# Performance work log

Measured on AMD Instinct MI355X. Metric: run time of the kernel, lower is better.

Reference implementation:

```python
import jax, jax.numpy as jnp
import numpy as np

EPS = 1e-6
DROPOUT_RATE = 0.1
NEG_INF = -1e9


def _rmsnorm(x, scale):
    # Llama2-style RMSNorm over the last (head_dim) axis.
    x_rms = jnp.sqrt((x * x).mean(axis=-1, keepdims=True) + EPS)
    return (x / x_rms) * scale


def setup_inputs() -> dict:
    key = jax.random.key(0)
    ks = jax.random.split(key, 5)
    B, S, H, D = 2, 2048, 16, 128
    query = jax.random.normal(ks[0], (B, S, H, D), dtype=jnp.float32)
    k_ = jax.random.normal(ks[1], (B, S, H, D), dtype=jnp.float32)
    value = jax.random.normal(ks[2], (B, S, H, D), dtype=jnp.float32)
    # Causal attention bias, broadcastable to [B, H, Sq, Sk].
    causal = jnp.tril(jnp.ones((S, S), dtype=bool))
    bias = jnp.where(causal, 0.0, NEG_INF).astype(jnp.float32)[None, None, :, :]
    q_scale = jnp.ones((D,), dtype=jnp.float32)
    k_scale = jnp.ones((D,), dtype=jnp.float32)
    # Dropout keep mask: broadcast over q dimension (dropout_shape[-2] = 1).
    keep_mask = jax.random.bernoulli(ks[3], 1.0 - DROPOUT_RATE, (B, H, 1, S))
    return {
        "query": query,
        "key": k_,
        "value": value,
        "bias": bias,
        "q_scale": q_scale,
        "k_scale": k_scale,
        "keep_mask": keep_mask,
    }


def reference(query, key, value, bias, q_scale, k_scale, keep_mask):
    # QK RMSNorm (maxtext applies RMSNorm to q and k inside attention).
    q = _rmsnorm(query, q_scale)  # [B, Sq, H, D]
    k = _rmsnorm(key, k_scale)    # [B, Sk, H, D]
    # Attention logits [B, H, Sq, Sk] (no 1/sqrt(d) scaling in this module).
    attn_weights = jnp.einsum("bqhd,bkhd->bhqk", q, k)
    attn_weights = attn_weights + bias.astype(attn_weights.dtype)
    attn_weights = jax.nn.softmax(attn_weights, axis=-1)
    # Dropout with keep mask broadcast over q length.
    keep_prob = 1.0 - DROPOUT_RATE
    multiplier = keep_mask.astype(attn_weights.dtype) / jnp.asarray(keep_prob, dtype=attn_weights.dtype)
    attn_weights = attn_weights * multiplier
    # Weighted value combine -> [B, Sq, H, D].
    return jnp.einsum("bhqk,bkhd->bqhd", attn_weights, value)
```

## Files before the change

kernel.cpp:

```cpp
#include <hip/hip_runtime.h>
#include <stdint.h>

typedef unsigned short u16;
typedef __attribute__((ext_vector_type(8))) _Float16 half8;
typedef __attribute__((ext_vector_type(4))) float f32x4;

#define DEVI __device__ __forceinline__

constexpr int B_ = 2, S_ = 2048, H_ = 16, D_ = 128;
constexpr int BH_ = B_ * H_;
constexpr float EPS_ = 1e-6f;
constexpr float INV_KEEP = 1.0f / 0.9f;

constexpr size_t Q_OFF = 0;
constexpr size_t K_OFF = (size_t)BH_ * S_ * D_ * 2;
constexpr size_t V_OFF = 2 * K_OFF;

DEVI u16 f16b(float x) { union { _Float16 f; u16 u; } c; c.f = (_Float16)x; return c.u; }

DEVI void gload16(const char* g, char* l) {
  __builtin_amdgcn_global_load_lds((const __attribute__((address_space(1))) uint32_t*)g,
                                   (__attribute__((address_space(3))) uint32_t*)l, 16, 0, 0);
}

__global__ __launch_bounds__(256) void k_norm(const float* __restrict__ q,
                                              const float* __restrict__ k,
                                              const float* __restrict__ qs,
                                              const float* __restrict__ ks,
                                              char* __restrict__ ws) {
  const int lane32 = threadIdx.x & 31;
  const int half = threadIdx.x >> 5;
  const float4 sq = *(const float4*)(qs + lane32 * 4);
  const float4 sk = *(const float4*)(ks + lane32 * 4);
  const int NROW = 2 * B_ * S_ * H_;

  for (int row = blockIdx.x * 8 + half; row < NROW; row += gridDim.x * 8) {
    const bool isQ = row < NROW / 2;
    const int r2 = isQ ? row : row - NROW / 2;
    const int b = r2 >> 15;
    const int s = (r2 >> 4) & (S_ - 1);
    const int h = r2 & 15;
    const float4 v = *(const float4*)((isQ ? q : k) + (size_t)r2 * D_ + lane32 * 4);
    float ss = v.x * v.x + v.y * v.y + v.z * v.z + v.w * v.w;
    ss += __shfl_xor(ss, 16); ss += __shfl_xor(ss, 8); ss += __shfl_xor(ss, 4);
    ss += __shfl_xor(ss, 2);  ss += __shfl_xor(ss, 1);
    const float f = rsqrtf(ss * (1.0f / D_) + EPS_);
    const float4 sc = isQ ? sq : sk;
    ushort4 o;
    o.x = f16b(v.x * f * sc.x); o.y = f16b(v.y * f * sc.y);
    o.z = f16b(v.z * f * sc.z); o.w = f16b(v.w * f * sc.w);
    const int bh = b * H_ + h;
    if (isQ) {
      *(ushort4*)(ws + Q_OFF + (((size_t)bh * S_ + s) * D_ + lane32 * 4) * 2) = o;
    } else {
      const int kt = s >> 6, r = s & 63;
      const int off = (r * 256 + lane32 * 8) ^ ((r & 7) << 4);
      *(ushort4*)(ws + K_OFF + ((size_t)(bh * 32 + kt) << 14) + off) = o;
    }
  }
}

__global__ __launch_bounds__(256) void k_vt(const float* __restrict__ v,
                                            const void* __restrict__ mask,
                                            char* __restrict__ ws) {
  __shared__ __align__(16) u16 tile[64][132];
  __shared__ float mlds[64];
  __shared__ int mode;

  const int bid = blockIdx.x;
  const int bh = bid >> 5, st = bid & 31;
  const int b = bh >> 4, h = bh & 15;
  const int t = threadIdx.x;

  if (t == 0) {
    const uint32_t* mw = (const uint32_t*)mask;
    bool all01 = true, allf = true;
    for (int i = 0; i < 64; i++) {
      uint32_t w = mw[i];
      if (w != 0u && w != 1u) all01 = false;
      if (w != 0u && w != 0x3F800000u) allf = false;
    }
    mode = all01 ? 1 : (allf ? 2 : 0);
  }
  __syncthreads();
  if (t < 64) {
    const int kidx = bh * S_ + st * 64 + t;
    int bit;
    if (mode == 1)      bit = ((const int*)mask)[kidx] != 0;
    else if (mode == 2) bit = ((const float*)mask)[kidx] != 0.0f;
    else                bit = ((const uint8_t*)mask)[kidx] != 0;
    mlds[t] = bit ? INV_KEEP : 0.0f;
  }
  __syncthreads();

  const int r = t >> 2, sub = t & 3;
  const size_t base = ((size_t)(b * S_ + st * 64 + r) * H_ + h) * D_;
  const float m = mlds[r];
  #pragma unroll
  for (int j = 0; j < 8; j++) {
    const int d = sub * 32 + j * 4;
    float4 val = *(const float4*)(v + base + d);
    ushort4 o;
    o.x = f16b(val.x * m); o.y = f16b(val.y * m);
    o.z = f16b(val.z * m); o.w = f16b(val.w * m);
    *(ushort4*)&tile[r][d] = o;
  }
  __syncthreads();

  const int dg = t >> 5;
  const int w = t & 31;
  char* tbase = ws + V_OFF + ((size_t)(bh * 32 + st) << 14);
  #pragma unroll
  for (int rr = 0; rr < 16; rr++) {
    const int d = rr * 8 + dg;
    const uint32_t word = (uint32_t)tile[2 * w][d] | ((uint32_t)tile[2 * w + 1][d] << 16);
    const int off = (d * 128 + w * 4) ^ ((d & 7) << 4);
    *(uint32_t*)(tbase + off) = word;
  }
}

__global__ __launch_bounds__(256, 2) void k_attn(const char* __restrict__ ws,
                                                 float* __restrict__ out) {
  __shared__ __align__(16) u16 K0[8192], V0[8192];
  __shared__ __align__(16) u16 K1[8192], V1[8192];
  __shared__ __align__(16) u16 Plds[4608];

  const int bid = blockIdx.x;
  const int bh = bid & 31, pair = bid >> 5;
  const int qtA = pair, qtB = 31 - pair;
  const int b = bh >> 4, h = bh & 15;
  const int t = threadIdx.x, wv = t >> 6, lane = t & 63;
  const int c = lane & 15, g = lane >> 4;

  half8 qA[4], qB[4];
  {
    const char* pA = ws + Q_OFF + (((size_t)bh * S_ + qtA * 64 + wv * 16 + c) * D_ + g * 8) * 2;
    const char* pB = ws + Q_OFF + (((size_t)bh * S_ + qtB * 64 + wv * 16 + c) * D_ + g * 8) * 2;
    #pragma unroll
    for (int kk = 0; kk < 4; kk++) {
      qA[kk] = *(const half8*)(pA + kk * 64);
      qB[kk] = *(const half8*)(pB + kk * 64);
    }
  }

  f32x4 accv[8];
  float mrun[4], lrun[4];
  #pragma unroll
  for (int i = 0; i < 8; i++) accv[i] = (f32x4){0.f, 0.f, 0.f, 0.f};
  #pragma unroll
  for (int r = 0; r < 4; r++) { mrun[r] = -1e30f; lrun[r] = 0.f; }

  const char* Kbase = ws + K_OFF + ((size_t)bh << 19);
  const char* Vbase = ws + V_OFF + ((size_t)bh << 19);
  const int nA = qtA + 1;
  constexpr int NIT = 33;

  auto stage = [&](int it, u16* lK, u16* lV) {
    const int kt = (it < nA) ? it : it - nA;
    const char* gk = Kbase + ((size_t)kt << 14) + wv * 4096 + lane * 16;
    const char* gv = Vbase + ((size_t)kt << 14) + wv * 4096 + lane * 16;
    char* lk = (char*)lK + wv * 4096;
    char* lv = (char*)lV + wv * 4096;
    #pragma unroll
    for (int j = 0; j < 4; j++) {
      gload16(gk + j * 1024, lk + j * 1024);
      gload16(gv + j * 1024, lv + j * 1024);
    }
  };

  auto dotile = [&](const half8 (&qf)[4], const u16* Kl, const u16* Vl, int kt, int qt) {
    f32x4 sacc[4];
    __builtin_amdgcn_s_setprio(1);
    #pragma unroll
    for (int tn = 0; tn < 4; tn++) {
      f32x4 s = (f32x4){0.f, 0.f, 0.f, 0.f};
      const int krow = tn * 16 + c;
      #pragma unroll
      for (int kk = 0; kk < 4; kk++) {
        const int byt = (krow * 256 + kk * 64 + g * 16) ^ ((krow & 7) << 4);
        half8 kf = *(const half8*)((const char*)Kl + byt);
        s = __builtin_amdgcn_mfma_f32_16x16x32_f16(qf[kk], kf, s, 0, 0, 0);
      }
      sacc[tn] = s;
    }
    __builtin_amdgcn_s_setprio(0);

    if (kt == qt) {
      #pragma unroll
      for (int tn = 0; tn < 4; tn++)
        #pragma unroll
        for (int r = 0; r < 4; r++)
          if (tn * 16 + c > wv * 16 + g * 4 + r) sacc[tn][r] = -1e30f;
    }

    float scl[4];
    #pragma unroll
    for (int r = 0; r < 4; r++) {
      float rm = fmaxf(fmaxf(sacc[0][r], sacc[1][r]), fmaxf(sacc[2][r], sacc[3][r]));
      rm = fmaxf(rm, __shfl_xor(rm, 1)); rm = fmaxf(rm, __shfl_xor(rm, 2));
      rm = fmaxf(rm, __shfl_xor(rm, 4)); rm = fmaxf(rm, __shfl_xor(rm, 8));
      const float mnew = fmaxf(mrun[r], rm);
      scl[r] = __expf(mrun[r] - mnew);
      mrun[r] = mnew;
      float rs = 0.f;
      #pragma unroll
      for (int tn = 0; tn < 4; tn++) {
        const float p = __expf(sacc[tn][r] - mnew);
        sacc[tn][r] = p;
        rs += p;
      }
      rs += __shfl_xor(rs, 1); rs += __shfl_xor(rs, 2);
      rs += __shfl_xor(rs, 4); rs += __shfl_xor(rs, 8);
      lrun[r] = lrun[r] * scl[r] + rs;
    }
    #pragma unroll
    for (int i = 0; i < 8; i++) {
      f32x4 a = accv[i];
      a[0] *= scl[0]; a[1] *= scl[1]; a[2] *= scl[2]; a[3] *= scl[3];
      accv[i] = a;
    }

    u16* Pw = Plds + wv * (16 * 72);
    #pragma unroll
    for (int tn = 0; tn < 4; tn++)
      #pragma unroll
      for (int r = 0; r < 4; r++)
        Pw[(g * 4 + r) * 72 + tn * 16 + c] = f16b(sacc[tn][r]);
    const half8 pf0 = *(const half8*)(Pw + c * 72 + g * 8);
    const half8 pf1 = *(const half8*)(Pw + c * 72 + 32 + g * 8);

    __builtin_amdgcn_s_setprio(1);
    #pragma unroll
    for (int dt = 0; dt < 8; dt++) {
      const int dcol = dt * 16 + c;
      const int b0 = (dcol * 128 + g * 16) ^ ((dcol & 7) << 4);
      const int b1 = (dcol * 128 + 64 + g * 16) ^ ((dcol & 7) << 4);
      half8 vf0 = *(const half8*)((const char*)Vl + b0);
      half8 vf1 = *(const half8*)((const char*)Vl + b1);
      accv[dt] = __builtin_amdgcn_mfma_f32_16x16x32_f16(pf0, vf0, accv[dt], 0, 0, 0);
      accv[dt] = __builtin_amdgcn_mfma_f32_16x16x32_f16(pf1, vf1, accv[dt], 0, 0, 0);
    }
    __builtin_amdgcn_s_setprio(0);
  };

  auto epil = [&](int qt) {
    float rl[4];
    #pragma unroll
    for (int r = 0; r < 4; r++) rl[r] = 1.0f / lrun[r];
    #pragma unroll
    for (int dt = 0; dt < 8; dt++)
      #pragma unroll
      for (int r = 0; r < 4; r++) {
        const int qq = qt * 64 + wv * 16 + g * 4 + r;
        out[((size_t)(b * S_ + qq) * H_ + h) * D_ + dt * 16 + c] = accv[dt][r] * rl[r];
      }
  };

  auto reset = [&]() {
    #pragma unroll
    for (int i = 0; i < 8; i++) accv[i] = (f32x4){0.f, 0.f, 0.f, 0.f};
    #pragma unroll
    for (int r = 0; r < 4; r++) { mrun[r] = -1e30f; lrun[r] = 0.f; }
  };

  stage(0, K0, V0);
  __syncthreads();
  int it = 0;
  while (true) {
    if (it + 1 < NIT) stage(it + 1, K1, V1);
    if (it < nA) dotile(qA, K0, V0, it, qtA);
    else         dotile(qB, K0, V0, it - nA, qtB);
    if (it == nA - 1) { epil(qtA); reset(); }
    __syncthreads();
    if (++it == NIT) break;

    if (it + 1 < NIT) stage(it + 1, K0, V0);
    if (it < nA) dotile(qA, K1, V1, it, qtA);
    else         dotile(qB, K1, V1, it - nA, qtB);
    if (it == nA - 1) { epil(qtA); reset(); }
    __syncthreads();
    if (++it == NIT) break;
  }
  epil(qtB);
}

extern "C" void kernel_launch(void* const* d_in, const int* in_sizes, int n_in,
                              void* d_out, int out_size, void* d_ws, size_t ws_size,
                              hipStream_t stream) {
  (void)in_sizes; (void)n_in; (void)out_size; (void)ws_size;
  const float* q  = (const float*)d_in[0];
  const float* k  = (const float*)d_in[1];
  const float* v  = (const float*)d_in[2];
  const float* qs = (const float*)d_in[4];
  const float* ks = (const float*)d_in[5];
  const void*  mk = d_in[6];
  float* out = (float*)d_out;
  char* ws = (char*)d_ws;

  k_norm<<<dim3(2048), dim3(256), 0, stream>>>(q, k, qs, ks, ws);
  k_vt<<<dim3(1024), dim3(256), 0, stream>>>(v, mk, ws);
  k_attn<<<dim3(512), dim3(256), 0, stream>>>(ws, out);
}
```

Before: 257.7 us.

## Enlarge attention tiles to 128x128 with 8 waves and transposed QK MFMA

Moves the attention kernel from 64-row to 128-row query and key tiles, using 512 threads per block (8 waves) and 256 blocks, and changes the K and V workspace layouts to match. The QK MFMA operands are swapped, so each lane holds one query row's scores. Row max and row sum then need fewer cross-lane shuffles, and the rescale factor is broadcast with shuffles. Larger tiles halve the loop iterations and barriers and double K/V reuse per LDS load. In exchange it uses 128KB+ of LDS per block, which lowers occupancy, and it halves the block count, which reduces parallelism across the GPU.

```diff
diff --git a/kernel.cpp b/kernel.cpp
--- a/kernel.cpp
+++ b/kernel.cpp
@@ -53,9 +53,9 @@
     if (isQ) {
       *(ushort4*)(ws + Q_OFF + (((size_t)bh * S_ + s) * D_ + lane32 * 4) * 2) = o;
     } else {
-      const int kt = s >> 6, r = s & 63;
+      const int kt = s >> 7, r = s & 127;
       const int off = (r * 256 + lane32 * 8) ^ ((r & 7) << 4);
-      *(ushort4*)(ws + K_OFF + ((size_t)(bh * 32 + kt) << 14) + off) = o;
+      *(ushort4*)(ws + K_OFF + ((size_t)(bh * 16 + kt) << 15) + off) = o;
     }
   }
 }
@@ -109,33 +109,35 @@
 
   const int dg = t >> 5;
   const int w = t & 31;
-  char* tbase = ws + V_OFF + ((size_t)(bh * 32 + st) << 14);
+  char* tbase = ws + V_OFF + ((size_t)(bh * 16 + (st >> 1)) << 15);
+  const int koff = (st & 1) * 128;
   #pragma unroll
   for (int rr = 0; rr < 16; rr++) {
     const int d = rr * 8 + dg;
     const uint32_t word = (uint32_t)tile[2 * w][d] | ((uint32_t)tile[2 * w + 1][d] << 16);
-    const int off = (d * 128 + w * 4) ^ ((d & 7) << 4);
+    const int off = (d * 256 + koff + w * 4) ^ ((d & 7) << 4);
     *(uint32_t*)(tbase + off) = word;
   }
 }
 
-__global__ __launch_bounds__(256, 2) void k_attn(const char* __restrict__ ws,
+__global__ __launch_bounds__(512, 2) void k_attn(const char* __restrict__ ws,
                                                  float* __restrict__ out) {
-  __shared__ __align__(16) u16 K0[8192], V0[8192];
-  __shared__ __align__(16) u16 K1[8192], V1[8192];
-  __shared__ __align__(16) u16 Plds[4608];
+  __shared__ __align__(16) char K0[32768], V0[32768];
+  __shared__ __align__(16) char K1[32768], V1[32768];
+  __shared__ __align__(16) u16 Plds[8 * 16 * 72];
 
   const int bid = blockIdx.x;
   const int bh = bid & 31, pair = bid >> 5;
-  const int qtA = pair, qtB = 31 - pair;
+  const int qtA = pair, qtB = 15 - pair;
   const int b = bh >> 4, h = bh & 15;
   const int t = threadIdx.x, wv = t >> 6, lane = t & 63;
   const int c = lane & 15, g = lane >> 4;
 
   half8 qA[4], qB[4];
   {
-    const char* pA = ws + Q_OFF + (((size_t)bh * S_ + qtA * 64 + wv * 16 + c) * D_ + g * 8) * 2;
-    const char* pB = ws + Q_OFF + (((size_t)bh * S_ + qtB * 64 + wv * 16 + c) * D_ + g * 8) * 2;
+    const char* Qb = ws + Q_OFF + (size_t)bh * S_ * D_ * 2;
+    const char* pA = Qb + (((size_t)qtA * 128 + wv * 16 + c) * D_ + g * 8) * 2;
+    const char* pB = Qb + (((size_t)qtB * 128 + wv * 16 + c) * D_ + g * 8) * 2;
     #pragma unroll
     for (int kk = 0; kk < 4; kk++) {
       qA[kk] = *(const half8*)(pA + kk * 64);
@@ -144,23 +146,21 @@
   }
 
   f32x4 accv[8];
-  float mrun[4], lrun[4];
   #pragma unroll
   for (int i = 0; i < 8; i++) accv[i] = (f32x4){0.f, 0.f, 0.f, 0.f};
-  #pragma unroll
-  for (int r = 0; r < 4; r++) { mrun[r] = -1e30f; lrun[r] = 0.f; }
+  float mrun = -1e30f, lrun = 0.f;
 
   const char* Kbase = ws + K_OFF + ((size_t)bh << 19);
   const char* Vbase = ws + V_OFF + ((size_t)bh << 19);
   const int nA = qtA + 1;
-  constexpr int NIT = 33;
-
-  auto stage = [&](int it, u16* lK, u16* lV) {
+  constexpr int NIT = 17;
+
+  auto stage = [&](int it, char* lK, char* lV) {
     const int kt = (it < nA) ? it : it - nA;
-    const char* gk = Kbase + ((size_t)kt << 14) + wv * 4096 + lane * 16;
-    const char* gv = Vbase + ((size_t)kt << 14) + wv * 4096 + lane * 16;
-    char* lk = (char*)lK + wv * 4096;
-    char* lv = (char*)lV + wv * 4096;
+    const char* gk = Kbase + ((size_t)kt << 15) + wv * 4096 + lane * 16;
+    const char* gv = Vbase + ((size_t)kt << 15) + wv * 4096 + lane * 16;
+    char* lk = lK + wv * 4096;
+    char* lv = lV + wv * 4096;
     #pragma unroll
     for (int j = 0; j < 4; j++) {
       gload16(gk + j * 1024, lk + j * 1024);
@@ -168,90 +168,100 @@
     }
   };
 
-  auto dotile = [&](const half8 (&qf)[4], const u16* Kl, const u16* Vl, int kt, int qt) {
-    f32x4 sacc[4];
+  auto dotile = [&](const half8 (&qf)[4], const char* Kl, const char* Vl, bool diag) {
+    f32x4 sacc[8];
     __builtin_amdgcn_s_setprio(1);
     #pragma unroll
-    for (int tn = 0; tn < 4; tn++) {
+    for (int tn = 0; tn < 8; tn++) {
       f32x4 s = (f32x4){0.f, 0.f, 0.f, 0.f};
       const int krow = tn * 16 + c;
       #pragma unroll
       for (int kk = 0; kk < 4; kk++) {
         const int byt = (krow * 256 + kk * 64 + g * 16) ^ ((krow & 7) << 4);
-        half8 kf = *(const half8*)((const char*)Kl + byt);
-        s = __builtin_amdgcn_mfma_f32_16x16x32_f16(qf[kk], kf, s, 0, 0, 0);
+        half8 kf = *(const half8*)(Kl + byt);
+        s = __builtin_amdgcn_mfma_f32_16x16x32_f16(kf, qf[kk], s, 0, 0, 0);
       }
       sacc[tn] = s;
     }
     __builtin_amdgcn_s_setprio(0);
 
-    if (kt == qt) {
-      #pragma unroll
-      for (int tn = 0; tn < 4; tn++)
+    if (diag) {
+      #pragma unroll
+      for (int tn = 0; tn < 8; tn++)
         #pragma unroll
         for (int r = 0; r < 4; r++)
-          if (tn * 16 + c > wv * 16 + g * 4 + r) sacc[tn][r] = -1e30f;
-    }
-
-    float scl[4];
-    #pragma unroll
-    for (int r = 0; r < 4; r++) {
-      float rm = fmaxf(fmaxf(sacc[0][r], sacc[1][r]), fmaxf(sacc[2][r], sacc[3][r]));
-      rm = fmaxf(rm, __shfl_xor(rm, 1)); rm = fmaxf(rm, __shfl_xor(rm, 2));
-      rm = fmaxf(rm, __shfl_xor(rm, 4)); rm = fmaxf(rm, __shfl_xor(rm, 8));
-      const float mnew = fmaxf(mrun[r], rm);
-      scl[r] = __expf(mrun[r] - mnew);
-      mrun[r] = mnew;
-      float rs = 0.f;
-      #pragma unroll
-      for (int tn = 0; tn < 4; tn++) {
+          if (tn * 16 + g * 4 + r > wv * 16 + c) sacc[tn][r] = -1e30f;
+    }
+
+    float pm = -1e30f;
+    #pragma unroll
+    for (int tn = 0; tn < 8; tn++)
+      pm = fmaxf(pm, fmaxf(fmaxf(sacc[tn][0], sacc[tn][1]),
+                           fmaxf(sacc[tn][2], sacc[tn][3])));
+    pm = fmaxf(pm, __shfl_xor(pm, 16));
+    pm = fmaxf(pm, __shfl_xor(pm, 32));
+    const float mnew = fmaxf(mrun, pm);
+    const float scl = __expf(mrun - mnew);
+    mrun = mnew;
+    float rs = 0.f;
+    #pragma unroll
+    for (int tn = 0; tn < 8; tn++) {
+      #pragma unroll
+      for (int r = 0; r < 4; r++) {
         const float p = __expf(sacc[tn][r] - mnew);
         sacc[tn][r] = p;
         rs += p;
       }
-      rs += __shfl_xor(rs, 1); rs += __shfl_xor(rs, 2);
-      rs += __shfl_xor(rs, 4); rs += __shfl_xor(rs, 8);
-      lrun[r] = lrun[r] * scl[r] + rs;
-    }
+    }
+    rs += __shfl_xor(rs, 16);
+    rs += __shfl_xor(rs, 32);
+    lrun = lrun * scl + rs;
+
+    float sa[4];
+    #pragma unroll
+    for (int r = 0; r < 4; r++) sa[r] = __shfl(scl, g * 4 + r);
     #pragma unroll
     for (int i = 0; i < 8; i++) {
       f32x4 a = accv[i];
-      a[0] *= scl[0]; a[1] *= scl[1]; a[2] *= scl[2]; a[3] *= scl[3];
+      a[0] *= sa[0]; a[1] *= sa[1]; a[2] *= sa[2]; a[3] *= sa[3];
       accv[i] = a;
     }
 
     u16* Pw = Plds + wv * (16 * 72);
     #pragma unroll
-    for (int tn = 0; tn < 4; tn++)
-      #pragma unroll
-      for (int r = 0; r < 4; r++)
-        Pw[(g * 4 + r) * 72 + tn * 16 + c] = f16b(sacc[tn][r]);
-    const half8 pf0 = *(const half8*)(Pw + c * 72 + g * 8);
-    const half8 pf1 = *(const half8*)(Pw + c * 72 + 32 + g * 8);
-
-    __builtin_amdgcn_s_setprio(1);
-    #pragma unroll
-    for (int dt = 0; dt < 8; dt++) {
-      const int dcol = dt * 16 + c;
-      const int b0 = (dcol * 128 + g * 16) ^ ((dcol & 7) << 4);
-      const int b1 = (dcol * 128 + 64 + g * 16) ^ ((dcol & 7) << 4);
-      half8 vf0 = *(const half8*)((const char*)Vl + b0);
-      half8 vf1 = *(const half8*)((const char*)Vl + b1);
-      accv[dt] = __builtin_amdgcn_mfma_f32_16x16x32_f16(pf0, vf0, accv[dt], 0, 0, 0);
-      accv[dt] = __builtin_amdgcn_mfma_f32_16x16x32_f16(pf1, vf1, accv[dt], 0, 0, 0);
-    }
-    __builtin_amdgcn_s_setprio(0);
+    for (int ph = 0; ph < 2; ph++) {
+      #pragma unroll
+      for (int tq = 0; tq < 4; tq++)
+        #pragma unroll
+        for (int r = 0; r < 4; r++)
+          Pw[c * 72 + tq * 16 + g * 4 + r] = f16b(sacc[ph * 4 + tq][r]);
+      const half8 pf0 = *(const half8*)(Pw + c * 72 + g * 8);
+      const half8 pf1 = *(const half8*)(Pw + c * 72 + 32 + g * 8);
+
+      __builtin_amdgcn_s_setprio(1);
+      #pragma unroll
+      for (int dt = 0; dt < 8; dt++) {
+        const int dcol = dt * 16 + c;
+        const int b0 = (dcol * 256 + ph * 128 + g * 16) ^ ((dcol & 7) << 4);
+        const int b1 = (dcol * 256 + ph * 128 + 64 + g * 16) ^ ((dcol & 7) << 4);
+        half8 vf0 = *(const half8*)(Vl + b0);
+        half8 vf1 = *(const half8*)(Vl + b1);
+        accv[dt] = __builtin_amdgcn_mfma_f32_16x16x32_f16(pf0, vf0, accv[dt], 0, 0, 0);
+        accv[dt] = __builtin_amdgcn_mfma_f32_16x16x32_f16(pf1, vf1, accv[dt], 0, 0, 0);
+      }
+      __builtin_amdgcn_s_setprio(0);
+    }
   };
 
-  auto epil = [&](int qt) {
+  auto epil = [&](int qsup) {
     float rl[4];
     #pragma unroll
-    for (int r = 0; r < 4; r++) rl[r] = 1.0f / lrun[r];
+    for (int r = 0; r < 4; r++) rl[r] = 1.0f / __shfl(lrun, g * 4 + r);
     #pragma unroll
     for (int dt = 0; dt < 8; dt++)
       #pragma unroll
       for (int r = 0; r < 4; r++) {
-        const int qq = qt * 64 + wv * 16 + g * 4 + r;
+        const int qq = qsup * 128 + wv * 16 + g * 4 + r;
         out[((size_t)(b * S_ + qq) * H_ + h) * D_ + dt * 16 + c] = accv[dt][r] * rl[r];
       }
   };
@@ -259,8 +269,7 @@
   auto reset = [&]() {
     #pragma unroll
     for (int i = 0; i < 8; i++) accv[i] = (f32x4){0.f, 0.f, 0.f, 0.f};
-    #pragma unroll
-    for (int r = 0; r < 4; r++) { mrun[r] = -1e30f; lrun[r] = 0.f; }
+    mrun = -1e30f; lrun = 0.f;
   };
 
   stage(0, K0, V0);
@@ -268,15 +277,15 @@
   int it = 0;
   while (true) {
     if (it + 1 < NIT) stage(it + 1, K1, V1);
-    if (it < nA) dotile(qA, K0, V0, it, qtA);
-    else         dotile(qB, K0, V0, it - nA, qtB);
+    if (it < nA) dotile(qA, K0, V0, it == nA - 1);
+    else         dotile(qB, K0, V0, it == NIT - 1);
     if (it == nA - 1) { epil(qtA); reset(); }
     __syncthreads();
     if (++it == NIT) break;
 
     if (it + 1 < NIT) stage(it + 1, K0, V0);
-    if (it < nA) dotile(qA, K1, V1, it, qtA);
-    else         dotile(qB, K1, V1, it - nA, qtB);
+    if (it < nA) dotile(qA, K1, V1, it == nA - 1);
+    else         dotile(qB, K1, V1, it == NIT - 1);
     if (it == nA - 1) { epil(qtA); reset(); }
     __syncthreads();
     if (++it == NIT) break;
@@ -299,5 +308,5 @@
 
   k_norm<<<dim3(2048), dim3(256), 0, stream>>>(q, k, qs, ks, ws);
   k_vt<<<dim3(1024), dim3(256), 0, stream>>>(v, mk, ws);
-  k_attn<<<dim3(512), dim3(256), 0, stream>>>(ws, out);
-}
+  k_attn<<<dim3(256), dim3(512), 0, stream>>>(ws, out);
+}
```

Measured after the change: 234.6 us. 9.0% less time.
